# Kernel tuning notes

Measured on AMD Instinct MI355X. Metric: run time of the kernel, lower is better.

## Reference

```python
import jax, jax.numpy as jnp
import numpy as np

B, IN_DIM, T = 4, 512, 4096
EMBED, HEADS, NB_FEAT = 1024, 16, 256
D_HEAD = EMBED // HEADS
EPS = 1e-6


def _orthogonal_random_matrix(key, nb_rows, nb_cols):
    # scaling==1 branch: sqrt(nb_cols) * Q from reduced QR of a Gaussian block
    block = jax.random.normal(key, (nb_rows, nb_cols), dtype=jnp.float32)
    q, _ = jnp.linalg.qr(block)
    return jnp.sqrt(jnp.float32(nb_cols)) * q


def setup_inputs() -> dict:
    key = jax.random.key(0)
    kx, kq, kk, kv, ko, kp = jax.random.split(key, 6)
    s = 1.0 / np.sqrt(IN_DIM)
    return {
        "x": jax.random.normal(kx, (B, IN_DIM, T), dtype=jnp.float32),
        "Wq": jax.random.normal(kq, (IN_DIM, EMBED), dtype=jnp.float32) * s,
        "Wk": jax.random.normal(kk, (IN_DIM, EMBED), dtype=jnp.float32) * s,
        "Wv": jax.random.normal(kv, (IN_DIM, EMBED), dtype=jnp.float32) * s,
        "Wo": jax.random.normal(ko, (EMBED, EMBED), dtype=jnp.float32) * (1.0 / np.sqrt(EMBED)),
        "proj": _orthogonal_random_matrix(kp, NB_FEAT, D_HEAD),
    }


def reference(x, Wq, Wk, Wv, Wo, proj):
    b, c, t = x.shape
    x_bt = jnp.transpose(x, (0, 2, 1))  # (B, T, in_dim)
    Q = (x_bt @ Wq).reshape(b, t, HEADS, D_HEAD)
    K = (x_bt @ Wk).reshape(b, t, HEADS, D_HEAD)
    V = (x_bt @ Wv).reshape(b, t, HEADS, D_HEAD)
    # exponential random-feature map
    Qp = jnp.exp(jnp.einsum('bthd,fd->bthf', Q, proj)) + EPS
    Kp = jnp.exp(jnp.einsum('bthd,fd->bthf', K, proj)) + EPS
    K_sum = Kp.sum(axis=1)                              # (B, H, F)
    KV = jnp.einsum('bthf,bthd->bhfd', Kp, V)           # (B, H, F, D)
    denom = jnp.maximum(jnp.einsum('bthf,bhf->bth', Qp, K_sum), 1e-6)
    numer = jnp.einsum('bthf,bhfd->bthd', Qp, KV)
    attn = numer / denom[..., None]                     # (B, T, H, D)
    out2 = attn.reshape(b, t, HEADS * D_HEAD) @ Wo      # (B, T, embed)
    cat = jnp.concatenate([x_bt, out2], axis=-1)        # (B, T, in_dim+embed)
    return jnp.transpose(cat, (0, 2, 1))
```

## Files before the change

kernel.cpp:

```cpp
#include <hip/hip_runtime.h>


constexpr int kB  = 4;
constexpr int kIn = 512;
constexpr int kT  = 4096;
constexpr int kE  = 1024;
constexpr int kH  = 16;
constexpr int kD  = 64;
constexpr int kF  = 256;
constexpr int kQKVs = 3072;

typedef __attribute__((ext_vector_type(8))) short bf16x8;
typedef __attribute__((ext_vector_type(4))) float f32x4;

__device__ __forceinline__ unsigned short f2bf(float f) {
    unsigned u = __float_as_uint(f);
    u += 0x7fff + ((u >> 16) & 1);
    return (unsigned short)(u >> 16);
}
__device__ __forceinline__ float bf2f(unsigned short s) {
    return __uint_as_float(((unsigned)s) << 16);
}
__device__ __forceinline__ void gload_lds16(const void* g, void* l) {
    __builtin_amdgcn_global_load_lds((const __attribute__((address_space(1))) void*)g,
                                     (__attribute__((address_space(3))) void*)l, 16, 0, 0);
}

__global__ __launch_bounds__(256) void zero_kernel(float* __restrict__ p, int n) {
    int i = blockIdx.x * 256 + threadIdx.x;
    if (i < n) p[i] = 0.f;
}

__global__ __launch_bounds__(256) void f2b_flat_kernel(const float* __restrict__ s,
                                                       unsigned short* __restrict__ d, int n4) {
    int i = blockIdx.x * 256 + threadIdx.x;
    if (i < n4) {
        float4 v = ((const float4*)s)[i];
        ushort4 o;
        o.x = f2bf(v.x); o.y = f2bf(v.y); o.z = f2bf(v.z); o.w = f2bf(v.w);
        ((ushort4*)d)[i] = o;
    }
}

__global__ __launch_bounds__(256) void trans_xcopy_kernel(const float* __restrict__ x,
                                                          float* __restrict__ out,
                                                          unsigned short* __restrict__ dst) {
    __shared__ float L[64][68];
    const int b = blockIdx.z;
    const float* src = x + (size_t)b * kIn * kT;
    float4* outb = (float4*)out + (size_t)b * ((kIn + kE) * kT / 4);
    unsigned short* dstb = dst + (size_t)b * kT * kIn;
    const int c0 = blockIdx.x * 64, r0 = blockIdx.y * 64;
    const int tid = threadIdx.x;
#pragma unroll
    for (int it = 0; it < 4; ++it) {
        int lin = it * 256 + tid;
        int i = lin >> 4;
        int j4 = (lin & 15) * 4;
        float4 v = *(const float4*)(src + (size_t)(r0 + i) * kT + c0 + j4);
        outb[((size_t)(r0 + i) * kT + c0 + j4) >> 2] = v;
        L[j4 + 0][i] = v.x; L[j4 + 1][i] = v.y; L[j4 + 2][i] = v.z; L[j4 + 3][i] = v.w;
    }
    __syncthreads();
#pragma unroll
    for (int it = 0; it < 4; ++it) {
        int lin = it * 256 + tid;
        int cc = lin >> 4;
        int r4 = (lin & 15) * 4;
        ushort4 o;
        o.x = f2bf(L[cc][r4 + 0]); o.y = f2bf(L[cc][r4 + 1]);
        o.z = f2bf(L[cc][r4 + 2]); o.w = f2bf(L[cc][r4 + 3]);
        *(ushort4*)(dstb + (size_t)(c0 + cc) * kIn + r0 + r4) = o;
    }
}

__global__ __launch_bounds__(256) void trans_f2b_kernel(const float* __restrict__ src,
                                                        unsigned short* __restrict__ dst,
                                                        int R, int C,
                                                        long sstride, long dstride) {
    __shared__ float L[64][68];
    src += (size_t)blockIdx.z * sstride;
    dst += (size_t)blockIdx.z * dstride;
    const int c0 = blockIdx.x * 64, r0 = blockIdx.y * 64;
    const int tid = threadIdx.x;
#pragma unroll
    for (int it = 0; it < 4; ++it) {
        int lin = it * 256 + tid;
        int i = lin >> 4;
        int j4 = (lin & 15) * 4;
        float4 v = *(const float4*)(src + (size_t)(r0 + i) * C + c0 + j4);
        L[j4 + 0][i] = v.x; L[j4 + 1][i] = v.y; L[j4 + 2][i] = v.z; L[j4 + 3][i] = v.w;
    }
    __syncthreads();
#pragma unroll
    for (int it = 0; it < 4; ++it) {
        int lin = it * 256 + tid;
        int cc = lin >> 4;
        int r4 = (lin & 15) * 4;
        ushort4 o;
        o.x = f2bf(L[cc][r4 + 0]); o.y = f2bf(L[cc][r4 + 1]);
        o.z = f2bf(L[cc][r4 + 2]); o.w = f2bf(L[cc][r4 + 3]);
        *(ushort4*)(dst + (size_t)(c0 + cc) * R + r0 + r4) = o;
    }
}

__global__ __launch_bounds__(256) void trans_qkv_kernel(const float* __restrict__ Wq,
                                                        const float* __restrict__ Wk,
                                                        const float* __restrict__ Wv,
                                                        unsigned short* __restrict__ dst) {
    __shared__ float L[64][68];
    const int z = blockIdx.z;
    const float* src = (z == 0) ? Wq : (z == 1) ? Wk : Wv;
    dst += (size_t)z * kE * kIn;
    const int c0 = blockIdx.x * 64, r0 = blockIdx.y * 64;
    const int tid = threadIdx.x;
#pragma unroll
    for (int it = 0; it < 4; ++it) {
        int lin = it * 256 + tid;
        int i = lin >> 4;
        int j4 = (lin & 15) * 4;
        float4 v = *(const float4*)(src + (size_t)(r0 + i) * kE + c0 + j4);
        L[j4 + 0][i] = v.x; L[j4 + 1][i] = v.y; L[j4 + 2][i] = v.z; L[j4 + 3][i] = v.w;
    }
    __syncthreads();
#pragma unroll
    for (int it = 0; it < 4; ++it) {
        int lin = it * 256 + tid;
        int cc = lin >> 4;
        int r4 = (lin & 15) * 4;
        ushort4 o;
        o.x = f2bf(L[cc][r4 + 0]); o.y = f2bf(L[cc][r4 + 1]);
        o.z = f2bf(L[cc][r4 + 2]); o.w = f2bf(L[cc][r4 + 3]);
        *(ushort4*)(dst + (size_t)(c0 + cc) * kIn + r0 + r4) = o;
    }
}

__device__ __forceinline__ void gemm128_mainloop(const unsigned short* __restrict__ A,
                                                 const unsigned short* __restrict__ Bt,
                                                 int K, int m0, int n0,
                                                 unsigned short* As, unsigned short* Bs,
                                                 f32x4 (&acc)[4][4]) {
    const int tid = threadIdx.x, lane = tid & 63, w = tid >> 6;
    const int col = lane & 15, quad = lane >> 4;
    const int wm = (w >> 2) * 64, wn = (w & 3) * 64;
    const int nt = K >> 5;

    const int srow = tid >> 2;
    const int schk = (tid & 3) ^ ((tid >> 3) & 3);
    const unsigned short* Agl  = A  + (size_t)(m0 + srow) * K + schk * 8;
    const unsigned short* Bgl0 = Bt + (size_t)(n0 + srow) * K + schk * 8;
    const unsigned short* Bgl1 = Bgl0 + (size_t)128 * K;
    unsigned short* Asw = As + w * 512;
    unsigned short* Bsw = Bs + w * 512;

    auto stage = [&](int kt, int buf) {
        gload_lds16(Agl  + kt * 32, Asw + buf * 4096);
        gload_lds16(Bgl0 + kt * 32, Bsw + buf * 8192);
        gload_lds16(Bgl1 + kt * 32, Bsw + buf * 8192 + 4096);
    };

#pragma unroll
    for (int i = 0; i < 4; ++i)
#pragma unroll
        for (int j = 0; j < 4; ++j) acc[i][j] = (f32x4){0.f, 0.f, 0.f, 0.f};

    stage(0, 0);
    if (nt > 1) stage(1, 1);
    asm volatile("s_waitcnt vmcnt(3)" ::: "memory");
    __builtin_amdgcn_s_barrier();
    __builtin_amdgcn_sched_barrier(0);

    const int rchk = (quad ^ ((col >> 1) & 3)) * 8;

    for (int t = 0; t < nt; ++t) {
        const int cur = t & 1;
        const unsigned short* Ab = As + cur * 4096;
        const unsigned short* Bb = Bs + cur * 8192;
        bf16x8 av[4], bv[4];
#pragma unroll
        for (int i = 0; i < 4; ++i)
            av[i] = *(const bf16x8*)&Ab[(wm + i * 16 + col) * 32 + rchk];
#pragma unroll
        for (int j = 0; j < 4; ++j)
            bv[j] = *(const bf16x8*)&Bb[(wn + j * 16 + col) * 32 + rchk];
        asm volatile("s_waitcnt lgkmcnt(0)" ::: "memory");
        __builtin_amdgcn_sched_barrier(0);
        __builtin_amdgcn_s_barrier();
        if (t + 2 < nt) stage(t + 2, cur);
        __builtin_amdgcn_sched_barrier(0);
#pragma unroll
        for (int i = 0; i < 4; ++i)
#pragma unroll
            for (int j = 0; j < 4; ++j)
                acc[i][j] = __builtin_amdgcn_mfma_f32_16x16x32_bf16(av[i], bv[j], acc[i][j], 0, 0, 0);
        if (t + 1 < nt) {
            __builtin_amdgcn_sched_barrier(0);
            if (t + 2 < nt) asm volatile("s_waitcnt vmcnt(3)" ::: "memory");
            else            asm volatile("s_waitcnt vmcnt(0)" ::: "memory");
            __builtin_amdgcn_sched_barrier(0);
            __builtin_amdgcn_s_barrier();
            __builtin_amdgcn_sched_barrier(0);
        }
    }
}

__global__ __launch_bounds__(512, 4) void gemm128_b16(const unsigned short* __restrict__ A,
                                                      const unsigned short* __restrict__ Bt,
                                                      unsigned short* __restrict__ C,
                                                      int N, int K, int ntN) {
    __shared__ unsigned short As[2 * 4096];
    __shared__ unsigned short Bs[2 * 8192];
    const int tid = threadIdx.x, lane = tid & 63, w = tid >> 6;
    const int col = lane & 15, quad = lane >> 4;
    const int wm = (w >> 2) * 64, wn = (w & 3) * 64;
    const int bid = blockIdx.x;
    const int qch = gridDim.x >> 3;
    const int swb = (bid & 7) * qch + (bid >> 3);
    const int mt = swb / ntN, ntl = swb - mt * ntN;
    const int m0 = mt * 128, n0 = ntl * 256;

    f32x4 acc[4][4];
    gemm128_mainloop(A, Bt, K, m0, n0, As, Bs, acc);

    float* Tw = (float*)As + w * 336;
    const int t2 = lane >> 2, n4 = (lane & 3) * 4;
#pragma unroll
    for (int ri = 0; ri < 4; ++ri)
#pragma unroll
        for (int cj = 0; cj < 4; ++cj) {
#pragma unroll
            for (int r = 0; r < 4; ++r)
                Tw[(quad * 4 + r) * 20 + col] = acc[ri][cj][r];
            float4 v = *(const float4*)&Tw[t2 * 20 + n4];
            ushort4 o;
            o.x = f2bf(v.x); o.y = f2bf(v.y); o.z = f2bf(v.z); o.w = f2bf(v.w);
            *(ushort4*)(C + (size_t)(m0 + wm + ri * 16 + t2) * N + n0 + wn + cj * 16 + n4) = o;
        }
}

__global__ __launch_bounds__(512, 4) void gemm128_out(const unsigned short* __restrict__ A,
                                                      const unsigned short* __restrict__ Bt,
                                                      float* __restrict__ out,
                                                      int N, int K, int ntN) {
    __shared__ unsigned short As[2 * 4096];
    __shared__ unsigned short Bs[2 * 8192];
    const int tid = threadIdx.x, lane = tid & 63, w = tid >> 6;
    const int col = lane & 15, quad = lane >> 4;
    const int wm = (w >> 2) * 64, wn = (w & 3) * 64;
    const int bid = blockIdx.x;
    const int qch = gridDim.x >> 3;
    const int swb = (bid & 7) * qch + (bid >> 3);
    const int mt = swb / ntN, ntl = swb - mt * ntN;
    const int m0 = mt * 128, n0 = ntl * 256;

    f32x4 acc[4][4];
    gemm128_mainloop(A, Bt, K, m0, n0, As, Bs, acc);

    const int b = m0 >> 12, t0 = m0 & 4095;
    float* dst = out + (size_t)b * (kIn + kE) * kT + (size_t)kIn * kT;
    float* Tw = (float*)As + w * 336;
    const int n2 = lane >> 2, t4 = (lane & 3) * 4;
#pragma unroll
    for (int ri = 0; ri < 4; ++ri)
#pragma unroll
        for (int cj = 0; cj < 4; ++cj) {
            *(float4*)&Tw[col * 20 + quad * 4] =
                (float4){acc[ri][cj][0], acc[ri][cj][1], acc[ri][cj][2], acc[ri][cj][3]};
            float4 v = *(const float4*)&Tw[n2 * 20 + t4];
            *(float4*)(dst + (size_t)(n0 + wn + cj * 16 + n2) * kT + t0 + wm + ri * 16 + t4) = v;
        }
}

__global__ __launch_bounds__(256) void phaseA_mfma(const unsigned short* __restrict__ QKVb,
                                                   const unsigned short* __restrict__ projb,
                                                   float* __restrict__ KVg,
                                                   float* __restrict__ Ksumg) {
    __shared__ unsigned short Ks[64 * 64];
    __shared__ unsigned short VT[64 * 72];
    __shared__ unsigned short KpT[256 * 72];
    const int tid = threadIdx.x, lane = tid & 63, w = tid >> 6;
    const int col = lane & 15, quad = lane >> 4;
    const int bh = blockIdx.x, b = bh >> 4, h = bh & 15;
    const int grp = blockIdx.y;
    const int f0 = w * 64;
    const int swz = col & 7;

    bf16x8 bB[2][4];
#pragma unroll
    for (int s = 0; s < 2; ++s)
#pragma unroll
        for (int j = 0; j < 4; ++j)
            bB[s][j] = *(const bf16x8*)(projb + (size_t)(f0 + j * 16 + col) * 64 + s * 32 + quad * 8);

    f32x4 kvacc[4][4];
#pragma unroll
    for (int i = 0; i < 4; ++i)
#pragma unroll
        for (int j = 0; j < 4; ++j) kvacc[i][j] = (f32x4){0.f, 0.f, 0.f, 0.f};
    float ksum_acc[4] = {0.f, 0.f, 0.f, 0.f};

    for (int it = 0; it < 4; ++it) {
        const size_t rowbase = (size_t)(b * kT + grp * 256 + it * 64) * kQKVs + h * kD;
        __syncthreads();
#pragma unroll
        for (int i2 = 0; i2 < 2; ++i2) {
            int p = (i2 * 4 + w) * 64 + lane;
            int row = p >> 3;
            int cg = ((p & 7) ^ (row & 7)) * 8;
            gload_lds16(QKVb + rowbase + 1024 + (size_t)row * kQKVs + cg, &Ks[(i2 * 4 + w) * 512]);
        }
#pragma unroll
        for (int r = 0; r < 4; ++r) {
            int lin = r * 256 + tid;
            int t = lin >> 4, d4 = (lin & 15) * 4;
            ushort4 v = *(const ushort4*)(QKVb + rowbase + 2048 + (size_t)t * kQKVs + d4);
            VT[(d4 + 0) * 72 + t] = v.x; VT[(d4 + 1) * 72 + t] = v.y;
            VT[(d4 + 2) * 72 + t] = v.z; VT[(d4 + 3) * 72 + t] = v.w;
        }
        __syncthreads();
        bf16x8 av[2][4];
#pragma unroll
        for (int s = 0; s < 2; ++s)
#pragma unroll
            for (int i = 0; i < 4; ++i)
                av[s][i] = *(const bf16x8*)&Ks[(i * 16 + col) * 64 + ((s * 4 + quad) ^ swz) * 8];
#pragma unroll
        for (int j = 0; j < 4; ++j) {
            f32x4 sa[4];
#pragma unroll
            for (int i = 0; i < 4; ++i) sa[i] = (f32x4){0.f, 0.f, 0.f, 0.f};
#pragma unroll
            for (int s = 0; s < 2; ++s)
#pragma unroll
                for (int i = 0; i < 4; ++i)
                    sa[i] = __builtin_amdgcn_mfma_f32_16x16x32_bf16(av[s][i], bB[s][j], sa[i], 0, 0, 0);
            const int f = f0 + j * 16 + col;
#pragma unroll
            for (int i = 0; i < 4; ++i) {
                float e0 = __expf(sa[i][0]) + 1e-6f;
                float e1 = __expf(sa[i][1]) + 1e-6f;
                float e2 = __expf(sa[i][2]) + 1e-6f;
                float e3 = __expf(sa[i][3]) + 1e-6f;
                ksum_acc[j] += (e0 + e1) + (e2 + e3);
                ushort4 pk;
                pk.x = f2bf(e0); pk.y = f2bf(e1); pk.z = f2bf(e2); pk.w = f2bf(e3);
                *(ushort4*)&KpT[f * 72 + i * 16 + quad * 4] = pk;
            }
        }
#pragma unroll
        for (int s = 0; s < 2; ++s) {
            const int kc = s * 32 + quad * 8;
            bf16x8 a2[4], b2[4];
#pragma unroll
            for (int i = 0; i < 4; ++i)
                a2[i] = *(const bf16x8*)&KpT[(f0 + i * 16 + col) * 72 + kc];
#pragma unroll
            for (int jn = 0; jn < 4; ++jn)
                b2[jn] = *(const bf16x8*)&VT[(jn * 16 + col) * 72 + kc];
#pragma unroll
            for (int i = 0; i < 4; ++i)
#pragma unroll
                for (int jn = 0; jn < 4; ++jn)
                    kvacc[i][jn] = __builtin_amdgcn_mfma_f32_16x16x32_bf16(a2[i], b2[jn], kvacc[i][jn], 0, 0, 0);
        }
    }
    const size_t kvbase = (size_t)bh * (kF * kD);
#pragma unroll
    for (int i = 0; i < 4; ++i)
#pragma unroll
        for (int jn = 0; jn < 4; ++jn)
#pragma unroll
            for (int r = 0; r < 4; ++r)
                atomicAdd(&KVg[kvbase + (size_t)(f0 + i * 16 + quad * 4 + r) * kD + jn * 16 + col],
                          kvacc[i][jn][r]);
#pragma unroll
    for (int j = 0; j < 4; ++j) {
        float v = ksum_acc[j];
        v += __shfl_xor(v, 16);
        v += __shfl_xor(v, 32);
        if (quad == 0) atomicAdd(&Ksumg[(size_t)bh * kF + f0 + j * 16 + col], v);
    }
}

__global__ __launch_bounds__(256) void phaseB_mfma(const unsigned short* __restrict__ QKVb,
                                                   const unsigned short* __restrict__ projb,
                                                   const unsigned short* __restrict__ KVTb,
                                                   const float* __restrict__ Ksumg,
                                                   unsigned short* __restrict__ attnb) {
    __shared__ unsigned short Qs[64 * 64];
    __shared__ unsigned short Qp[64 * 264];
    __shared__ unsigned short KVTs[64 * 264];
    __shared__ float KsS[256];
    __shared__ float denp[4][64];
    const int tid = threadIdx.x, lane = tid & 63, w = tid >> 6;
    const int col = lane & 15, quad = lane >> 4;
    const int bh = blockIdx.x, b = bh >> 4, h = bh & 15;
    const int grp = blockIdx.y;
    const int f0 = w * 64;
    const int swz = col & 7;

    bf16x8 bB[2][4];
#pragma unroll
    for (int s = 0; s < 2; ++s)
#pragma unroll
        for (int j = 0; j < 4; ++j)
            bB[s][j] = *(const bf16x8*)(projb + (size_t)(f0 + j * 16 + col) * 64 + s * 32 + quad * 8);

#pragma unroll
    for (int r = 0; r < 8; ++r) {
        int lin = r * 256 + tid;
        int d = lin >> 5, fc8 = (lin & 31) * 8;
        *(bf16x8*)&KVTs[d * 264 + fc8] = *(const bf16x8*)(KVTb + (size_t)bh * 16384 + d * 256 + fc8);
    }
    KsS[tid] = Ksumg[(size_t)bh * kF + tid];

    for (int it = 0; it < 8; ++it) {
        const int tg0 = grp * 512 + it * 64;
        const size_t rowbase = (size_t)(b * kT + tg0) * kQKVs + h * kD;
        __syncthreads();
#pragma unroll
        for (int i2 = 0; i2 < 2; ++i2) {
            int p = (i2 * 4 + w) * 64 + lane;
            int row = p >> 3;
            int cg = ((p & 7) ^ (row & 7)) * 8;
            gload_lds16(QKVb + rowbase + (size_t)row * kQKVs + cg, &Qs[(i2 * 4 + w) * 512]);
        }
        __syncthreads();
        bf16x8 av[2][4];
#pragma unroll
        for (int s = 0; s < 2; ++s)
#pragma unroll
            for (int i = 0; i < 4; ++i)
                av[s][i] = *(const bf16x8*)&Qs[(i * 16 + col) * 64 + ((s * 4 + quad) ^ swz) * 8];
#pragma unroll
        for (int j = 0; j < 4; ++j) {
            f32x4 sa[4];
#pragma unroll
            for (int i = 0; i < 4; ++i) sa[i] = (f32x4){0.f, 0.f, 0.f, 0.f};
#pragma unroll
            for (int s = 0; s < 2; ++s)
#pragma unroll
                for (int i = 0; i < 4; ++i)
                    sa[i] = __builtin_amdgcn_mfma_f32_16x16x32_bf16(av[s][i], bB[s][j], sa[i], 0, 0, 0);
            const int f = f0 + j * 16 + col;
#pragma unroll
            for (int i = 0; i < 4; ++i) {
                const int tb = i * 16 + quad * 4;
                Qp[(tb + 0) * 264 + f] = f2bf(__expf(sa[i][0]) + 1e-6f);
                Qp[(tb + 1) * 264 + f] = f2bf(__expf(sa[i][1]) + 1e-6f);
                Qp[(tb + 2) * 264 + f] = f2bf(__expf(sa[i][2]) + 1e-6f);
                Qp[(tb + 3) * 264 + f] = f2bf(__expf(sa[i][3]) + 1e-6f);
            }
        }
        float dp = 0.f;
#pragma unroll
        for (int u = 0; u < 64; u += 8) {
            bf16x8 qv = *(const bf16x8*)&Qp[lane * 264 + f0 + u];
#pragma unroll
            for (int k2 = 0; k2 < 8; ++k2)
                dp += bf2f((unsigned short)qv[k2]) * KsS[f0 + u + k2];
        }
        denp[w][lane] = dp;
        __syncthreads();
        f32x4 nacc[4];
#pragma unroll
        for (int jn = 0; jn < 4; ++jn) nacc[jn] = (f32x4){0.f, 0.f, 0.f, 0.f};
#pragma unroll
        for (int s = 0; s < 8; ++s) {
            const int kc = s * 32 + quad * 8;
            bf16x8 aq = *(const bf16x8*)&Qp[(w * 16 + col) * 264 + kc];
#pragma unroll
            for (int jn = 0; jn < 4; ++jn) {
                bf16x8 bk = *(const bf16x8*)&KVTs[(jn * 16 + col) * 264 + kc];
                nacc[jn] = __builtin_amdgcn_mfma_f32_16x16x32_bf16(aq, bk, nacc[jn], 0, 0, 0);
            }
        }
#pragma unroll
        for (int r = 0; r < 4; ++r) {
            const int tl = w * 16 + quad * 4 + r;
            float den = denp[0][tl] + denp[1][tl] + denp[2][tl] + denp[3][tl];
            float rd = 1.f / fmaxf(den, 1e-6f);
            const size_t ob = (size_t)(b * kT + tg0 + tl) * kE + h * kD;
#pragma unroll
            for (int jn = 0; jn < 4; ++jn)
                attnb[ob + jn * 16 + col] = f2bf(nacc[jn][r] * rd);
        }
    }
}

extern "C" void kernel_launch(void* const* d_in, const int* in_sizes, int n_in,
                              void* d_out, int out_size, void* d_ws, size_t ws_size,
                              hipStream_t stream) {
    (void)in_sizes; (void)n_in; (void)out_size; (void)ws_size;
    const float* x    = (const float*)d_in[0];
    const float* Wq   = (const float*)d_in[1];
    const float* Wk   = (const float*)d_in[2];
    const float* Wv   = (const float*)d_in[3];
    const float* Wo   = (const float*)d_in[4];
    const float* proj = (const float*)d_in[5];
    float* out = (float*)d_out;

    char* ws = (char*)d_ws;
    unsigned short* QKVb  = (unsigned short*)(ws);
    unsigned short* attnb = (unsigned short*)(ws + 100663296);
    unsigned short* Abuf  = (unsigned short*)(ws + 100663296);
    unsigned short* Btqkv = (unsigned short*)(ws + 134217728);
    unsigned short* WoT   = (unsigned short*)(ws + 137363456);
    unsigned short* projb = (unsigned short*)(ws + 139460608);
    float*          KVg   = (float*)(ws + 139493376);
    float*          Ksumg = (float*)(ws + 143687680);
    unsigned short* KVTb  = (unsigned short*)(ws + 143753216);

    trans_xcopy_kernel<<<dim3(64, 8, 4), 256, 0, stream>>>(x, out, Abuf);
    trans_qkv_kernel<<<dim3(16, 8, 3), 256, 0, stream>>>(Wq, Wk, Wv, Btqkv);
    trans_f2b_kernel<<<dim3(16, 16, 1), 256, 0, stream>>>(Wo, WoT, kE, kE, 0, 0);
    f2b_flat_kernel<<<dim3(16), 256, 0, stream>>>(proj, projb, kF * kD / 4);

    gemm128_b16<<<dim3(1536), 512, 0, stream>>>(Abuf, Btqkv, QKVb, kQKVs, kIn, 12);

    const int nz = kB * kH * kF * kD + kB * kH * kF;
    zero_kernel<<<dim3((nz + 255) / 256), 256, 0, stream>>>(KVg, nz);

    phaseA_mfma<<<dim3(64, 16), 256, 0, stream>>>(QKVb, projb, KVg, Ksumg);
    trans_f2b_kernel<<<dim3(1, 4, 64), 256, 0, stream>>>(KVg, KVTb, kF, kD,
                                                         (long)kF * kD, (long)kF * kD);
    phaseB_mfma<<<dim3(64, 8), 256, 0, stream>>>(QKVb, projb, KVTb, Ksumg, attnb);

    gemm128_out<<<dim3(512), 512, 0, stream>>>(attnb, WoT, out, kE, kE, 4);
}
```

Baseline: 378.3 us.

## Double-buffer K/V tile loads in phaseA and halve grid to 8 chunks

```diff
diff --git a/kernel.cpp b/kernel.cpp
--- a/kernel.cpp
+++ b/kernel.cpp
@@ -275,7 +275,7 @@
                                                    const unsigned short* __restrict__ projb,
                                                    float* __restrict__ KVg,
                                                    float* __restrict__ Ksumg) {
-    __shared__ unsigned short Ks[64 * 64];
+    __shared__ unsigned short Ks[2 * 4096];
     __shared__ unsigned short VT[64 * 72];
     __shared__ unsigned short KpT[256 * 72];
     const int tid = threadIdx.x, lane = tid & 63, w = tid >> 6;
@@ -285,6 +285,14 @@
     const int f0 = w * 64;
     const int swz = col & 7;
 
+    const int p0 = w * 64 + lane, p1 = (4 + w) * 64 + lane;
+    const int krow0 = p0 >> 3, kcg0 = ((p0 & 7) ^ (krow0 & 7)) * 8;
+    const int krow1 = p1 >> 3, kcg1 = ((p1 & 7) ^ (krow1 & 7)) * 8;
+    const int vt_t = tid >> 4, vd4 = (tid & 15) * 4;
+    const int vsw = (vd4 >> 2) & 7;
+
+    const size_t base0 = (size_t)(b * kT + grp * 512) * kQKVs + h * kD;
+
     bf16x8 bB[2][4];
 #pragma unroll
     for (int s = 0; s < 2; ++s)
@@ -299,31 +307,50 @@
         for (int j = 0; j < 4; ++j) kvacc[i][j] = (f32x4){0.f, 0.f, 0.f, 0.f};
     float ksum_acc[4] = {0.f, 0.f, 0.f, 0.f};
 
-    for (int it = 0; it < 4; ++it) {
-        const size_t rowbase = (size_t)(b * kT + grp * 256 + it * 64) * kQKVs + h * kD;
-        __syncthreads();
-#pragma unroll
-        for (int i2 = 0; i2 < 2; ++i2) {
-            int p = (i2 * 4 + w) * 64 + lane;
-            int row = p >> 3;
-            int cg = ((p & 7) ^ (row & 7)) * 8;
-            gload_lds16(QKVb + rowbase + 1024 + (size_t)row * kQKVs + cg, &Ks[(i2 * 4 + w) * 512]);
-        }
+    ushort4 vrA[4], vrB[4];
+
+    auto kissue = [&](int it, int buf) {
+        const size_t rb = base0 + (size_t)(it * 64) * kQKVs + 1024;
+        gload_lds16(QKVb + rb + (size_t)krow0 * kQKVs + kcg0, &Ks[buf * 4096 + w * 512]);
+        gload_lds16(QKVb + rb + (size_t)krow1 * kQKVs + kcg1, &Ks[buf * 4096 + (4 + w) * 512]);
+    };
+    auto vload = [&](int it, ushort4* vr) {
+        const size_t rb = base0 + (size_t)(it * 64) * kQKVs + 2048;
+#pragma unroll
+        for (int r = 0; r < 4; ++r)
+            vr[r] = *(const ushort4*)(QKVb + rb + (size_t)(r * 16 + vt_t) * kQKVs + vd4);
+    };
+    auto vtwrite = [&](const ushort4* vr) {
 #pragma unroll
         for (int r = 0; r < 4; ++r) {
-            int lin = r * 256 + tid;
-            int t = lin >> 4, d4 = (lin & 15) * 4;
-            ushort4 v = *(const ushort4*)(QKVb + rowbase + 2048 + (size_t)t * kQKVs + d4);
-            VT[(d4 + 0) * 72 + t] = v.x; VT[(d4 + 1) * 72 + t] = v.y;
-            VT[(d4 + 2) * 72 + t] = v.z; VT[(d4 + 3) * 72 + t] = v.w;
-        }
-        __syncthreads();
+            const int t = r * 16 + vt_t;
+            const int bo = (((t >> 3) ^ vsw) * 8) + (t & 7);
+            VT[(vd4 + 0) * 72 + bo] = vr[r].x;
+            VT[(vd4 + 1) * 72 + bo] = vr[r].y;
+            VT[(vd4 + 2) * 72 + bo] = vr[r].z;
+            VT[(vd4 + 3) * 72 + bo] = vr[r].w;
+        }
+    };
+
+    kissue(0, 0); vload(0, vrA);
+    kissue(1, 1); vload(1, vrB);
+    asm volatile("s_waitcnt vmcnt(6)" ::: "memory");
+    __builtin_amdgcn_sched_barrier(0);
+    vtwrite(vrA);
+    asm volatile("s_waitcnt lgkmcnt(0)" ::: "memory");
+    __builtin_amdgcn_sched_barrier(0);
+    __builtin_amdgcn_s_barrier();
+    __builtin_amdgcn_sched_barrier(0);
+
+#pragma unroll 2
+    for (int it = 0; it < 8; ++it) {
+        const int cur = it & 1;
         bf16x8 av[2][4];
 #pragma unroll
         for (int s = 0; s < 2; ++s)
 #pragma unroll
             for (int i = 0; i < 4; ++i)
-                av[s][i] = *(const bf16x8*)&Ks[(i * 16 + col) * 64 + ((s * 4 + quad) ^ swz) * 8];
+                av[s][i] = *(const bf16x8*)&Ks[cur * 4096 + (i * 16 + col) * 64 + ((s * 4 + quad) ^ swz) * 8];
 #pragma unroll
         for (int j = 0; j < 4; ++j) {
             f32x4 sa[4];
@@ -355,15 +382,36 @@
             for (int i = 0; i < 4; ++i)
                 a2[i] = *(const bf16x8*)&KpT[(f0 + i * 16 + col) * 72 + kc];
 #pragma unroll
-            for (int jn = 0; jn < 4; ++jn)
-                b2[jn] = *(const bf16x8*)&VT[(jn * 16 + col) * 72 + kc];
+            for (int jn = 0; jn < 4; ++jn) {
+                const int d = jn * 16 + col;
+                b2[jn] = *(const bf16x8*)&VT[d * 72 + (((s * 4 + quad) ^ ((d >> 2) & 7)) * 8)];
+            }
 #pragma unroll
             for (int i = 0; i < 4; ++i)
 #pragma unroll
                 for (int jn = 0; jn < 4; ++jn)
                     kvacc[i][jn] = __builtin_amdgcn_mfma_f32_16x16x32_bf16(a2[i], b2[jn], kvacc[i][jn], 0, 0, 0);
         }
-    }
+        if (it < 7) {
+            __builtin_amdgcn_sched_barrier(0);
+            __builtin_amdgcn_s_barrier();
+            __builtin_amdgcn_sched_barrier(0);
+            if (it < 6) {
+                kissue(it + 2, cur);
+                vload(it + 2, (it & 1) ? vrB : vrA);
+                asm volatile("s_waitcnt vmcnt(6)" ::: "memory");
+            } else {
+                asm volatile("s_waitcnt vmcnt(0)" ::: "memory");
+            }
+            __builtin_amdgcn_sched_barrier(0);
+            vtwrite((it & 1) ? vrA : vrB);
+            asm volatile("s_waitcnt lgkmcnt(0)" ::: "memory");
+            __builtin_amdgcn_sched_barrier(0);
+            __builtin_amdgcn_s_barrier();
+            __builtin_amdgcn_sched_barrier(0);
+        }
+    }
+
     const size_t kvbase = (size_t)bh * (kF * kD);
 #pragma unroll
     for (int i = 0; i < 4; ++i)
@@ -521,7 +569,7 @@
     const int nz = kB * kH * kF * kD + kB * kH * kF;
     zero_kernel<<<dim3((nz + 255) / 256), 256, 0, stream>>>(KVg, nz);
 
-    phaseA_mfma<<<dim3(64, 16), 256, 0, stream>>>(QKVb, projb, KVg, Ksumg);
+    phaseA_mfma<<<dim3(64, 8), 256, 0, stream>>>(QKVb, projb, KVg, Ksumg);
     trans_f2b_kernel<<<dim3(1, 4, 64), 256, 0, stream>>>(KVg, KVTb, kF, kD,
                                                          (long)kF * kD, (long)kF * kD);
     phaseB_mfma<<<dim3(64, 8), 256, 0, stream>>>(QKVb, projb, KVTb, Ksumg, attnb);
```

Result: faster. 360.2 us (-4.8%).

## Replace atomic KV accumulation with per-group partials and a reduce kernel

Applied to the files above, without the earlier changes.

```diff
diff --git a/kernel.cpp b/kernel.cpp
--- a/kernel.cpp
+++ b/kernel.cpp
@@ -9,6 +9,7 @@
 constexpr int kD  = 64;
 constexpr int kF  = 256;
 constexpr int kQKVs = 3072;
+constexpr int kNG  = 8;
 
 typedef __attribute__((ext_vector_type(8))) short bf16x8;
 typedef __attribute__((ext_vector_type(4))) float f32x4;
@@ -24,11 +25,6 @@
 __device__ __forceinline__ void gload_lds16(const void* g, void* l) {
     __builtin_amdgcn_global_load_lds((const __attribute__((address_space(1))) void*)g,
                                      (__attribute__((address_space(3))) void*)l, 16, 0, 0);
-}
-
-__global__ __launch_bounds__(256) void zero_kernel(float* __restrict__ p, int n) {
-    int i = blockIdx.x * 256 + threadIdx.x;
-    if (i < n) p[i] = 0.f;
 }
 
 __global__ __launch_bounds__(256) void f2b_flat_kernel(const float* __restrict__ s,
@@ -132,6 +128,38 @@
         o.x = f2bf(L[cc][r4 + 0]); o.y = f2bf(L[cc][r4 + 1]);
         o.z = f2bf(L[cc][r4 + 2]); o.w = f2bf(L[cc][r4 + 3]);
         *(ushort4*)(dst + (size_t)(c0 + cc) * kIn + r0 + r4) = o;
+    }
+}
+
+__global__ __launch_bounds__(256) void kv_reduce_kernel(const float* __restrict__ KVp,
+                                                        unsigned short* __restrict__ KVTb) {
+    __shared__ float L[64][68];
+    const int r0 = blockIdx.x * 64;
+    const int bh = blockIdx.y;
+    const int tid = threadIdx.x;
+#pragma unroll
+    for (int it = 0; it < 4; ++it) {
+        int lin = it * 256 + tid;
+        int i = lin >> 4;
+        int j4 = (lin & 15) * 4;
+        float4 s = {0.f, 0.f, 0.f, 0.f};
+#pragma unroll
+        for (int g = 0; g < kNG; ++g) {
+            float4 v = *(const float4*)(KVp + ((size_t)(g * 64 + bh) * 256 + r0 + i) * 64 + j4);
+            s.x += v.x; s.y += v.y; s.z += v.z; s.w += v.w;
+        }
+        L[j4 + 0][i] = s.x; L[j4 + 1][i] = s.y; L[j4 + 2][i] = s.z; L[j4 + 3][i] = s.w;
+    }
+    __syncthreads();
+#pragma unroll
+    for (int it = 0; it < 4; ++it) {
+        int lin = it * 256 + tid;
+        int cc = lin >> 4;
+        int r4 = (lin & 15) * 4;
+        ushort4 o;
+        o.x = f2bf(L[cc][r4 + 0]); o.y = f2bf(L[cc][r4 + 1]);
+        o.z = f2bf(L[cc][r4 + 2]); o.w = f2bf(L[cc][r4 + 3]);
+        *(ushort4*)(KVTb + (size_t)bh * 16384 + (size_t)cc * kF + r0 + r4) = o;
     }
 }
 
@@ -273,8 +301,8 @@
 
 __global__ __launch_bounds__(256) void phaseA_mfma(const unsigned short* __restrict__ QKVb,
                                                    const unsigned short* __restrict__ projb,
-                                                   float* __restrict__ KVg,
-                                                   float* __restrict__ Ksumg) {
+                                                   float* __restrict__ KVp,
+                                                   float* __restrict__ Ksump) {
     __shared__ unsigned short Ks[64 * 64];
     __shared__ unsigned short VT[64 * 72];
     __shared__ unsigned short KpT[256 * 72];
@@ -285,6 +313,9 @@
     const int f0 = w * 64;
     const int swz = col & 7;
 
+    const int vt_t = tid >> 4, vd4 = (tid & 15) * 4;
+    const int vsw = (vd4 >> 2) & 7;
+
     bf16x8 bB[2][4];
 #pragma unroll
     for (int s = 0; s < 2; ++s)
@@ -299,8 +330,8 @@
         for (int j = 0; j < 4; ++j) kvacc[i][j] = (f32x4){0.f, 0.f, 0.f, 0.f};
     float ksum_acc[4] = {0.f, 0.f, 0.f, 0.f};
 
-    for (int it = 0; it < 4; ++it) {
-        const size_t rowbase = (size_t)(b * kT + grp * 256 + it * 64) * kQKVs + h * kD;
+    for (int it = 0; it < 8; ++it) {
+        const size_t rowbase = (size_t)(b * kT + grp * 512 + it * 64) * kQKVs + h * kD;
         __syncthreads();
 #pragma unroll
         for (int i2 = 0; i2 < 2; ++i2) {
@@ -309,13 +340,18 @@
             int cg = ((p & 7) ^ (row & 7)) * 8;
             gload_lds16(QKVb + rowbase + 1024 + (size_t)row * kQKVs + cg, &Ks[(i2 * 4 + w) * 512]);
         }
+        ushort4 vr[4];
+#pragma unroll
+        for (int r = 0; r < 4; ++r)
+            vr[r] = *(const ushort4*)(QKVb + rowbase + 2048 + (size_t)(r * 16 + vt_t) * kQKVs + vd4);
 #pragma unroll
         for (int r = 0; r < 4; ++r) {
-            int lin = r * 256 + tid;
-            int t = lin >> 4, d4 = (lin & 15) * 4;
-            ushort4 v = *(const ushort4*)(QKVb + rowbase + 2048 + (size_t)t * kQKVs + d4);
-            VT[(d4 + 0) * 72 + t] = v.x; VT[(d4 + 1) * 72 + t] = v.y;
-            VT[(d4 + 2) * 72 + t] = v.z; VT[(d4 + 3) * 72 + t] = v.w;
+            const int t = r * 16 + vt_t;
+            const int bo = (((t >> 3) ^ vsw) * 8) + (t & 7);
+            VT[(vd4 + 0) * 72 + bo] = vr[r].x;
+            VT[(vd4 + 1) * 72 + bo] = vr[r].y;
+            VT[(vd4 + 2) * 72 + bo] = vr[r].z;
+            VT[(vd4 + 3) * 72 + bo] = vr[r].w;
         }
         __syncthreads();
         bf16x8 av[2][4];
@@ -355,8 +391,10 @@
             for (int i = 0; i < 4; ++i)
                 a2[i] = *(const bf16x8*)&KpT[(f0 + i * 16 + col) * 72 + kc];
 #pragma unroll
-            for (int jn = 0; jn < 4; ++jn)
-                b2[jn] = *(const bf16x8*)&VT[(jn * 16 + col) * 72 + kc];
+            for (int jn = 0; jn < 4; ++jn) {
+                const int d = jn * 16 + col;
+                b2[jn] = *(const bf16x8*)&VT[d * 72 + (((s * 4 + quad) ^ ((d >> 2) & 7)) * 8)];
+            }
 #pragma unroll
             for (int i = 0; i < 4; ++i)
 #pragma unroll
@@ -364,28 +402,27 @@
                     kvacc[i][jn] = __builtin_amdgcn_mfma_f32_16x16x32_bf16(a2[i], b2[jn], kvacc[i][jn], 0, 0, 0);
         }
     }
-    const size_t kvbase = (size_t)bh * (kF * kD);
+    float* dst = KVp + (size_t)(grp * 64 + bh) * 16384;
 #pragma unroll
     for (int i = 0; i < 4; ++i)
 #pragma unroll
         for (int jn = 0; jn < 4; ++jn)
 #pragma unroll
             for (int r = 0; r < 4; ++r)
-                atomicAdd(&KVg[kvbase + (size_t)(f0 + i * 16 + quad * 4 + r) * kD + jn * 16 + col],
-                          kvacc[i][jn][r]);
+                dst[(size_t)(f0 + i * 16 + quad * 4 + r) * kD + jn * 16 + col] = kvacc[i][jn][r];
 #pragma unroll
     for (int j = 0; j < 4; ++j) {
         float v = ksum_acc[j];
         v += __shfl_xor(v, 16);
         v += __shfl_xor(v, 32);
-        if (quad == 0) atomicAdd(&Ksumg[(size_t)bh * kF + f0 + j * 16 + col], v);
+        if (quad == 0) Ksump[(size_t)(grp * 64 + bh) * kF + f0 + j * 16 + col] = v;
     }
 }
 
 __global__ __launch_bounds__(256) void phaseB_mfma(const unsigned short* __restrict__ QKVb,
                                                    const unsigned short* __restrict__ projb,
                                                    const unsigned short* __restrict__ KVTb,
-                                                   const float* __restrict__ Ksumg,
+                                                   const float* __restrict__ Ksump,
                                                    unsigned short* __restrict__ attnb) {
     __shared__ unsigned short Qs[64 * 64];
     __shared__ unsigned short Qp[64 * 264];
@@ -412,7 +449,13 @@
         int d = lin >> 5, fc8 = (lin & 31) * 8;
         *(bf16x8*)&KVTs[d * 264 + fc8] = *(const bf16x8*)(KVTb + (size_t)bh * 16384 + d * 256 + fc8);
     }
-    KsS[tid] = Ksumg[(size_t)bh * kF + tid];
+    {
+        float s = 0.f;
+#pragma unroll
+        for (int g = 0; g < kNG; ++g)
+            s += Ksump[(size_t)(g * 64 + bh) * kF + tid];
+        KsS[tid] = s;
+    }
 
     for (int it = 0; it < 8; ++it) {
         const int tg0 = grp * 512 + it * 64;
@@ -504,11 +547,11 @@
     unsigned short* QKVb  = (unsigned short*)(ws);
     unsigned short* attnb = (unsigned short*)(ws + 100663296);
     unsigned short* Abuf  = (unsigned short*)(ws + 100663296);
+    float*          KVp   = (float*)(ws + 100663296);
     unsigned short* Btqkv = (unsigned short*)(ws + 134217728);
     unsigned short* WoT   = (unsigned short*)(ws + 137363456);
     unsigned short* projb = (unsigned short*)(ws + 139460608);
-    float*          KVg   = (float*)(ws + 139493376);
-    float*          Ksumg = (float*)(ws + 143687680);
+    float*          Ksump = (float*)(ws + 139493376);
     unsigned short* KVTb  = (unsigned short*)(ws + 143753216);
 
     trans_xcopy_kernel<<<dim3(64, 8, 4), 256, 0, stream>>>(x, out, Abuf);
@@ -518,13 +561,9 @@
 
     gemm128_b16<<<dim3(1536), 512, 0, stream>>>(Abuf, Btqkv, QKVb, kQKVs, kIn, 12);
 
-    const int nz = kB * kH * kF * kD + kB * kH * kF;
-    zero_kernel<<<dim3((nz + 255) / 256), 256, 0, stream>>>(KVg, nz);
-
-    phaseA_mfma<<<dim3(64, 16), 256, 0, stream>>>(QKVb, projb, KVg, Ksumg);
-    trans_f2b_kernel<<<dim3(1, 4, 64), 256, 0, stream>>>(KVg, KVTb, kF, kD,
-                                                         (long)kF * kD, (long)kF * kD);
-    phaseB_mfma<<<dim3(64, 8), 256, 0, stream>>>(QKVb, projb, KVTb, Ksumg, attnb);
+    phaseA_mfma<<<dim3(64, kNG), 256, 0, stream>>>(QKVb, projb, KVp, Ksump);
+    kv_reduce_kernel<<<dim3(4, 64), 256, 0, stream>>>(KVp, KVTb);
+    phaseB_mfma<<<dim3(64, 8), 256, 0, stream>>>(QKVb, projb, KVTb, Ksump, attnb);
 
     gemm128_out<<<dim3(512), 512, 0, stream>>>(attnb, WoT, out, kE, kE, 4);
 }
```

Result: faster. 355.4 us (-6.1%).
